# Kernel tuning notes

Hardware: AMD Instinct MI355X
Metric: run time of the kernel (lower is better)

## Reference

```python
import jax, jax.numpy as jnp
import numpy as np

NUM_GAUSS = 64
MAX_R = 5.0
ANG_TO_NM = 0.1  # du.ANG_TO_NM_SCALE
L = 4
C_NODE = 256
C_HID = 256
MAX_ATOMS = 100
B = 512      # building blocks
NPB = 32     # atoms per block
K = 20       # max_neighbors
N = B * NPB
E = N * K
GAUSS_COEFF = -0.5 / (MAX_R / (NUM_GAUSS - 1)) ** 2


def setup_inputs() -> dict:
    rng = np.random.default_rng(0)
    # all atoms of a block inside a 2.5A cube -> every pair within MAX_R=5A,
    # so radius_graph capped at K neighbors == K-nearest graph (fixed E).
    pos = (rng.random((B, NPB, 3)) * 2.5).astype(np.float32)
    d = np.linalg.norm(pos[:, :, None, :] - pos[:, None, :, :], axis=-1)  # [B,n,n]
    ii = np.arange(NPB)
    d[:, ii, ii] = np.inf  # loop=False
    nbr = np.argsort(d, axis=-1)[:, :, :K]  # [B,n,K] nearest neighbors
    base = (np.arange(B) * NPB)[:, None, None]
    row = np.broadcast_to(ii[None, :, None], (B, NPB, K)) + base
    col = nbr + base
    edge_index = np.stack([row.reshape(-1), col.reshape(-1)]).astype(np.int64)

    key = jax.random.key(0)
    ks = jax.random.split(key, 8)

    def lin(k, fi, fo):
        return jax.random.normal(k, (L, fi, fo), jnp.float32) / np.sqrt(fi).astype(np.float32)

    d_e_in = 2 * C_NODE + 1 + NUM_GAUSS  # 577
    return {
        'local_coords': jnp.asarray(pos.reshape(N, 3)),
        'atom_types': jax.random.randint(ks[0], (N,), 1, MAX_ATOMS + 1),  # 1..max_atoms
        'edge_index': jnp.asarray(edge_index),
        'batch_bb': jnp.repeat(jnp.arange(B, dtype=jnp.int32), NPB),
        'atom_embed': jax.random.normal(ks[1], (MAX_ATOMS, C_NODE), jnp.float32) * 0.1,
        'offset': jnp.linspace(0.0, MAX_R, NUM_GAUSS, dtype=jnp.float32),
        'We1': lin(ks[2], d_e_in, C_HID), 'be1': jnp.zeros((L, C_HID), jnp.float32),
        'We2': lin(ks[3], C_HID, C_HID), 'be2': jnp.zeros((L, C_HID), jnp.float32),
        'Wn1': lin(ks[4], C_HID + C_NODE, C_HID), 'bn1': jnp.zeros((L, C_HID), jnp.float32),
        'Wn2': lin(ks[5], C_HID, C_NODE), 'bn2': jnp.zeros((L, C_NODE), jnp.float32),
    }


def _forward(local_coords, atom_types, edge_index, batch_bb, atom_embed, offset,
             We1, be1, We2, be2, Wn1, bn1, Wn2, bn2):
    row, col = edge_index[0], edge_index[1]
    h = atom_embed[atom_types - 1]                      # [N, C_NODE]
    # Gaussian smearing of pairwise distances (Angstrom)
    dvec = local_coords[col] - local_coords[row]        # [E, 3]
    dist = jnp.sqrt(jnp.sum(dvec * dvec, axis=-1))      # [E]
    edge_attr = jnp.exp(GAUSS_COEFF * (dist[:, None] - offset[None, :]) ** 2)  # [E, 64]
    coord = local_coords * ANG_TO_NM
    cdiff = coord[row] - coord[col]
    radial = jnp.sum(cdiff * cdiff, axis=-1, keepdims=True)  # [E, 1]
    nblocks = batch_bb.shape[0] // NPB  # static
    for l in range(L):  # small fixed layer count
        e_in = jnp.concatenate([h[row], h[col], radial, edge_attr], axis=-1)  # [E, 577]
        m = jax.nn.relu(e_in @ We1[l] + be1[l])
        m = jax.nn.relu(m @ We2[l] + be2[l])                 # edge_mlp output [E, C_HID]
        agg = jax.ops.segment_sum(m, row, num_segments=N)    # scatter-sum to nodes
        n_in = jnp.concatenate([h, agg], axis=-1)            # [N, C_NODE + C_HID]
        out = jax.nn.relu(n_in @ Wn1[l] + bn1[l]) @ Wn2[l] + bn2[l]
        node_update = h + out                                # residual inside E_GCL
        h = h + node_update                                  # outer residual in forward
    # global_mean_pool over building blocks
    s = jax.ops.segment_sum(h, batch_bb, num_segments=B)
    cnt = jax.ops.segment_sum(jnp.ones((h.shape[0], 1), h.dtype), batch_bb, num_segments=B)
    return s / cnt


def reference(local_coords, atom_types, edge_index, batch_bb, atom_embed, offset,
              We1, be1, We2, be2, Wn1, bn1, Wn2, bn2):
    return _forward(local_coords, atom_types, edge_index, batch_bb, atom_embed, offset,
                    We1, be1, We2, be2, Wn1, bn1, Wn2, bn2)
```

## Files before the change

kernel.cpp:

```cpp
#include <hip/hip_runtime.h>
#include <hip/hip_bf16.h>
#include <stdint.h>

#define NATOMS 16384
#define ETOT   327680
#define NLAYER 4

typedef __hip_bfloat16 bf16;
using bf16x8 = __attribute__((ext_vector_type(8))) short;
using bf16x4 = __attribute__((ext_vector_type(4))) short;
using f32x4  = __attribute__((ext_vector_type(4))) float;

#define LDSF_STRIDE 260

__device__ __forceinline__ float bf2f(short s) {
  union { float f; unsigned u; } x; x.u = ((unsigned)(unsigned short)s) << 16; return x.f;
}
__device__ __forceinline__ short f2bf(float f) {
  bf16 b = __float2bfloat16(f);
  return *(short*)&b;
}

__device__ __forceinline__ void async16(const void* g, void* l) {
  __builtin_amdgcn_global_load_lds(
      (const __attribute__((address_space(1))) unsigned int*)g,
      (__attribute__((address_space(3))) unsigned int*)l, 16, 0, 0);
}

template<int KTOT, int EPI, int MT>
__global__ void __launch_bounds__(256, 2)
gemm_k(const bf16* A, const bf16* A2, const bf16* B,
       bf16* Obf, int ldOut, const float* bias,
       float* Hf, bf16* Hbf)
{
  __shared__ __align__(16) char smem[49152];
  const int tid  = threadIdx.x;
  const int w    = tid >> 6;
  const int lane = tid & 63;
  const int q    = lane >> 4;
  const int t16  = lane & 15;
  const size_t row0 = (size_t)blockIdx.x * MT;
  const int ncol0 = blockIdx.y * 256;
  constexpr int MI = MT / 16;
  constexpr int AI = MT / 32;

  f32x4 acc[MI][4] = {};
  constexpr int NCHUNK = KTOT / 64;
  for (int kc = 0; kc < NCHUNK; ++kc) {
    const int k0 = kc * 64;
    __syncthreads();
    #pragma unroll
    for (int ii = 0; ii < AI; ++ii) {
      int i = w * AI + ii;
      int f = i * 64 + lane;
      int m = f >> 3, s = f & 7;
      int ko = s ^ (m & 7);
      async16(A + (row0 + (size_t)m) * KTOT + (size_t)(k0 + ko * 8), smem + i * 1024);
    }
    #pragma unroll
    for (int ii = 0; ii < 8; ++ii) {
      int i = w * 8 + ii;
      int f = i * 64 + lane;
      int n = f >> 3, s = f & 7;
      int ko = s ^ (n & 7);
      async16(B + (size_t)(ncol0 + n) * KTOT + (size_t)(k0 + ko * 8),
              smem + 16384 + i * 1024);
    }
    __syncthreads();
    #pragma unroll
    for (int ks = 0; ks < 2; ++ks) {
      bf16x8 av[MI]; bf16x8 bv[4];
      const int ko = q + 4 * ks;
      #pragma unroll
      for (int mi = 0; mi < MI; ++mi) {
        int m = 16 * mi + t16;
        int f = m * 8 + (ko ^ (m & 7));
        av[mi] = *(const bf16x8*)(smem + f * 16);
      }
      #pragma unroll
      for (int ni = 0; ni < 4; ++ni) {
        int n = 64 * w + 16 * ni + t16;
        int f = n * 8 + (ko ^ (n & 7));
        bv[ni] = *(const bf16x8*)(smem + 16384 + f * 16);
      }
      #pragma unroll
      for (int mi = 0; mi < MI; ++mi)
        #pragma unroll
        for (int ni = 0; ni < 4; ++ni)
          acc[mi][ni] = __builtin_amdgcn_mfma_f32_16x16x32_bf16(
              av[mi], bv[ni], acc[mi][ni], 0, 0, 0);
    }
  }

  float* lds_f = (float*)smem;
  #pragma unroll
  for (int mi = 0; mi < MI; ++mi) {
    __syncthreads();
    #pragma unroll
    for (int ni = 0; ni < 4; ++ni)
      #pragma unroll
      for (int r = 0; r < 4; ++r)
        lds_f[(4 * q + r) * LDSF_STRIDE + 64 * w + 16 * ni + t16] = acc[mi][ni][r];
    __syncthreads();
    #pragma unroll
    for (int j = 0; j < 2; ++j) {
      int task = tid + 256 * j;
      int rr = task >> 5, cg = task & 31;
      int c0 = cg * 8;
      size_t rg = row0 + 16 * mi + rr;
      f32x4 v0 = *(const f32x4*)(lds_f + rr * LDSF_STRIDE + c0);
      f32x4 v1 = *(const f32x4*)(lds_f + rr * LDSF_STRIDE + c0 + 4);
      float v[8] = {v0[0], v0[1], v0[2], v0[3], v1[0], v1[1], v1[2], v1[3]};
      bf16x8 o;
      #pragma unroll
      for (int k = 0; k < 8; ++k) {
        float vv = v[k];
        if (bias != nullptr && ncol0 == 0) vv += bias[c0 + k];
        o[k] = f2bf(vv);
      }
      *(bf16x8*)(Obf + rg * ldOut + (ncol0 + c0)) = o;
    }
  }
}

#define WINC 40960
#define WINR 57856
#define SCOL 59968
#define SRAD 60288
#define WPITCH 528

__global__ void __launch_bounds__(256, 2)
edge_fused(const bf16* Wgp_l, const bf16* W2p_l, const float* off,
           const float* pos, const int* eidx, const bf16* Prc,
           const float* wrad, const float* be2, bf16* Agg)
{
  __shared__ __align__(16) char smem[60608];
  int*   s_col = (int*)  (smem + SCOL);
  float* s_rad = (float*)(smem + SRAD);

  const int tid  = threadIdx.x;
  const int w    = tid >> 6;
  const int lane = tid & 63;
  const int q    = lane >> 4;
  const int t16  = lane & 15;
  const int blk  = blockIdx.x;
  const int node0  = (blk >> 3) * 32;
  const int rnode0 = blk * 4;
  const int ebase  = blk * 80;

  bf16x8 wgf[4][2];
  #pragma unroll
  for (int fi = 0; fi < 4; ++fi)
    #pragma unroll
    for (int ks = 0; ks < 2; ++ks)
      wgf[fi][ks] = *(const bf16x8*)(Wgp_l + (size_t)(((fi * 2 + ks) * 4 + w) * 512)
                                     + lane * 8);

  {
    int row = tid >> 3, seg = tid & 7;
    const bf16* src = Prc + (size_t)(node0 + row) * 512 + 256 + seg * 32;
    char* dst = smem + WINC + row * WPITCH + seg * 64;
    #pragma unroll
    for (int j = 0; j < 4; ++j)
      *(bf16x8*)(dst + j * 16) = *(const bf16x8*)(src + j * 8);
  }
  if (tid < 128) {
    int row = tid >> 5, seg = tid & 31;
    *(bf16x8*)(smem + WINR + row * WPITCH + seg * 16) =
        *(const bf16x8*)(Prc + (size_t)(rnode0 + row) * 512 + seg * 8);
  }

  if (tid < 80) {
    int e = ebase + tid;
    int rg = rnode0 + tid / 20;
    int cg = eidx[ETOT + e];
    float dx = pos[cg * 3 + 0] - pos[rg * 3 + 0];
    float dy = pos[cg * 3 + 1] - pos[rg * 3 + 1];
    float dz = pos[cg * 3 + 2] - pos[rg * 3 + 2];
    float d2 = dx * dx + dy * dy + dz * dz;
    s_col[tid] = cg & 31;
    s_rad[tid] = 0.01f * d2;
    float d = sqrtf(d2);
    const float GC = -0.5f / ((5.0f / 63.0f) * (5.0f / 63.0f));
    #pragma unroll
    for (int oct = 0; oct < 8; ++oct) {
      bf16x8 v;
      #pragma unroll
      for (int j = 0; j < 8; ++j) {
        float t = d - off[oct * 8 + j];
        v[j] = f2bf(__expf(GC * t * t));
      }
      int f = tid * 8 + (oct ^ (tid & 7));
      *(bf16x8*)(smem + f * 16) = v;
    }
  }
  __syncthreads();

  f32x4 acc1[4][5] = {};
  #pragma unroll
  for (int ks = 0; ks < 2; ++ks) {
    const int ko = q + 4 * ks;
    bf16x8 gv[5];
    #pragma unroll
    for (int ci = 0; ci < 5; ++ci) {
      int e = 16 * ci + t16;
      int f = e * 8 + (ko ^ (e & 7));
      gv[ci] = *(const bf16x8*)(smem + f * 16);
    }
    #pragma unroll
    for (int fi = 0; fi < 4; ++fi)
      #pragma unroll
      for (int ci = 0; ci < 5; ++ci)
        acc1[fi][ci] = __builtin_amdgcn_mfma_f32_16x16x32_bf16(
            wgf[fi][ks], gv[ci], acc1[fi][ci], 0, 0, 0);
  }
  __syncthreads();

  {
    f32x4 tw[4];
    #pragma unroll
    for (int fi = 0; fi < 4; ++fi)
      tw[fi] = *(const f32x4*)(wrad + 64 * w + 16 * fi + 4 * q);
    #pragma unroll
    for (int ci = 0; ci < 5; ++ci) {
      int e = 16 * ci + t16;
      int rl = e / 20;
      int cl = s_col[e];
      float rad = s_rad[e];
      #pragma unroll
      for (int fi = 0; fi < 4; ++fi) {
        int fb = 64 * w + 16 * fi + 4 * q;
        bf16x4 pr = *(const bf16x4*)(smem + WINR + rl * WPITCH + fb * 2);
        bf16x4 pc = *(const bf16x4*)(smem + WINC + cl * WPITCH + fb * 2);
        bf16x4 o;
        #pragma unroll
        for (int r = 0; r < 4; ++r) {
          float val = acc1[fi][ci][r] + rad * tw[fi][r]
                    + bf2f(pr[r]) + bf2f(pc[r]);
          o[r] = f2bf(fmaxf(val, 0.f));
        }
        int u = (16 * w + 4 * fi + q) ^ (e & 14);
        *(bf16x4*)(smem + e * 512 + u * 8) = o;
      }
    }
  }
  __syncthreads();

  f32x4 acc2[5][4] = {};
  #pragma unroll
  for (int kc = 0; kc < 4; ++kc) {
    bf16x8 bv[4][2];
    #pragma unroll
    for (int ni = 0; ni < 4; ++ni)
      #pragma unroll
      for (int ks = 0; ks < 2; ++ks) {
        int frag = kc * 8 + ks * 4 + ni;
        bv[ni][ks] = *(const bf16x8*)(W2p_l + (size_t)((frag * 4 + w) * 512)
                                      + lane * 8);
      }
    #pragma unroll
    for (int ks = 0; ks < 2; ++ks) {
      const int ko = q + 4 * ks;
      bf16x8 av[5];
      #pragma unroll
      for (int mi = 0; mi < 5; ++mi) {
        int e = 16 * mi + t16;
        int ub = (2 * (8 * kc + ko)) ^ (t16 & 14);
        av[mi] = *(const bf16x8*)(smem + e * 512 + ub * 8);
      }
      #pragma unroll
      for (int mi = 0; mi < 5; ++mi)
        #pragma unroll
        for (int ni = 0; ni < 4; ++ni)
          acc2[mi][ni] = __builtin_amdgcn_mfma_f32_16x16x32_bf16(
              av[mi], bv[ni][ks], acc2[mi][ni], 0, 0, 0);
    }
  }

  #pragma unroll
  for (int ni = 0; ni < 4; ++ni) {
    float b = be2[64 * w + 16 * ni + t16];
    float pp[5];
    #pragma unroll
    for (int mi = 0; mi < 5; ++mi) {
      float s = 0.f;
      #pragma unroll
      for (int r = 0; r < 4; ++r) s += fmaxf(acc2[mi][ni][r] + b, 0.f);
      pp[mi] = s;
    }
    #pragma unroll
    for (int nn = 0; nn < 4; ++nn) {
      float s = 0.f;
      #pragma unroll
      for (int mi = 0; mi < 5; ++mi) {
        int g = 4 * mi + q;
        if (g >= 5 * nn && g <= 5 * nn + 4) s += pp[mi];
      }
      s += __shfl_xor(s, 16, 64);
      s += __shfl_xor(s, 32, 64);
      if (q == nn)
        Agg[(size_t)(rnode0 + nn) * 256 + 64 * w + 16 * ni + t16] =
            __float2bfloat16(s);
    }
  }
}

template<bool DO_PRC>
__global__ void __launch_bounds__(256, 2)
node_fused(const bf16* Hbf_in, const bf16* Agg, const bf16* Wn1p_l,
           const bf16* Wn2p_l, const bf16* Wrcp_n,
           const float* bn1, const float* bn2, const float* be1_n,
           float* Hf, bf16* Hbf, bf16* Prc)
{
  __shared__ __align__(16) char smem[49152];
  __shared__ float s_bn1[256];
  __shared__ float s_bn2[256];
  char* T = smem + 32768;
  float* lds_f = (float*)smem;

  const int tid  = threadIdx.x;
  const int w    = tid >> 6;
  const int lane = tid & 63;
  const int q    = lane >> 4;
  const int t16  = lane & 15;
  const size_t row0 = (size_t)blockIdx.x * 32;

  #pragma unroll
  for (int ii = 0; ii < 8; ++ii) {
    int i = w * 8 + ii;
    int ko = (lane & 56) | ((lane & 7) ^ (i & 7));
    const bf16* srcp = ((lane < 32) ? Hbf_in : Agg)
                     + (row0 + (size_t)i) * 256 + ((ko * 8) & 255);
    async16(srcp, smem + i * 1024);
  }
  s_bn1[tid] = bn1[tid];
  s_bn2[tid] = bn2[tid];
  __syncthreads();

  f32x4 acc1[4][2] = {};
  for (int kc = 0; kc < 8; ++kc) {
    #pragma unroll
    for (int ks = 0; ks < 2; ++ks) {
      const int ko = kc * 8 + q + 4 * ks;
      bf16x8 af[4];
      #pragma unroll
      for (int fi = 0; fi < 4; ++fi)
        af[fi] = *(const bf16x8*)(Wn1p_l +
                   (size_t)((fi * 16 + kc * 2 + ks) * 4 + w) * 512 + lane * 8);
      bf16x8 bv[2];
      #pragma unroll
      for (int ci = 0; ci < 2; ++ci) {
        int node = 16 * ci + t16;
        int sl = (ko & 56) | ((ko & 7) ^ (node & 7));
        bv[ci] = *(const bf16x8*)(smem + node * 1024 + sl * 16);
      }
      #pragma unroll
      for (int fi = 0; fi < 4; ++fi)
        #pragma unroll
        for (int ci = 0; ci < 2; ++ci)
          acc1[fi][ci] = __builtin_amdgcn_mfma_f32_16x16x32_bf16(
              af[fi], bv[ci], acc1[fi][ci], 0, 0, 0);
    }
  }

  #pragma unroll
  for (int ci = 0; ci < 2; ++ci) {
    int node = 16 * ci + t16;
    #pragma unroll
    for (int fi = 0; fi < 4; ++fi) {
      int fb = 64 * w + 16 * fi + 4 * q;
      f32x4 tb = *(const f32x4*)(s_bn1 + fb);
      bf16x4 o;
      #pragma unroll
      for (int r = 0; r < 4; ++r)
        o[r] = f2bf(fmaxf(acc1[fi][ci][r] + tb[r], 0.f));
      int u = (16 * w + 4 * fi + q) ^ (node & 14);
      *(bf16x4*)(T + node * 512 + u * 8) = o;
    }
  }
  __syncthreads();

  f32x4 acc2[2][4] = {};
  #pragma unroll
  for (int kc = 0; kc < 4; ++kc) {
    bf16x8 bv[4][2];
    #pragma unroll
    for (int ni = 0; ni < 4; ++ni)
      #pragma unroll
      for (int ks = 0; ks < 2; ++ks) {
        int frag = kc * 8 + ks * 4 + ni;
        bv[ni][ks] = *(const bf16x8*)(Wn2p_l + (size_t)((frag * 4 + w) * 512)
                                      + lane * 8);
      }
    #pragma unroll
    for (int ks = 0; ks < 2; ++ks) {
      const int ko = q + 4 * ks;
      bf16x8 av[2];
      #pragma unroll
      for (int mi = 0; mi < 2; ++mi) {
        int row = 16 * mi + t16;
        int ub = (2 * (8 * kc + ko)) ^ (t16 & 14);
        av[mi] = *(const bf16x8*)(T + row * 512 + ub * 8);
      }
      #pragma unroll
      for (int mi = 0; mi < 2; ++mi)
        #pragma unroll
        for (int ni = 0; ni < 4; ++ni)
          acc2[mi][ni] = __builtin_amdgcn_mfma_f32_16x16x32_bf16(
              av[mi], bv[ni][ks], acc2[mi][ni], 0, 0, 0);
    }
  }

  #pragma unroll
  for (int mi = 0; mi < 2; ++mi) {
    __syncthreads();
    #pragma unroll
    for (int ni = 0; ni < 4; ++ni)
      #pragma unroll
      for (int r = 0; r < 4; ++r)
        lds_f[(4 * q + r) * LDSF_STRIDE + 64 * w + 16 * ni + t16] = acc2[mi][ni][r];
    __syncthreads();
    #pragma unroll
    for (int j = 0; j < 2; ++j) {
      int task = tid + 256 * j;
      int rr = task >> 5, cg = task & 31;
      int c0 = cg * 8;
      int rl = 16 * mi + rr;
      size_t rg = row0 + rl;
      f32x4 v0 = *(const f32x4*)(lds_f + rr * LDSF_STRIDE + c0);
      f32x4 v1 = *(const f32x4*)(lds_f + rr * LDSF_STRIDE + c0 + 4);
      float v[8] = {v0[0], v0[1], v0[2], v0[3], v1[0], v1[1], v1[2], v1[3]};
      f32x4 h0 = *(const f32x4*)(Hf + rg * 256 + c0);
      f32x4 h1 = *(const f32x4*)(Hf + rg * 256 + c0 + 4);
      float hh[8] = {h0[0], h0[1], h0[2], h0[3], h1[0], h1[1], h1[2], h1[3]};
      bf16x8 o; f32x4 n0, n1;
      #pragma unroll
      for (int k = 0; k < 8; ++k) {
        float hn = 2.f * hh[k] + v[k] + s_bn2[c0 + k];
        o[k] = f2bf(hn);
        if (k < 4) n0[k] = hn; else n1[k - 4] = hn;
      }
      *(f32x4*)(Hf + rg * 256 + c0)     = n0;
      *(f32x4*)(Hf + rg * 256 + c0 + 4) = n1;
      *(bf16x8*)(Hbf + rg * 256 + c0) = o;
      int s = cg ^ ((rl >> 1) & 7);
      *(bf16x8*)(T + rl * 512 + s * 16) = o;
    }
  }

  if constexpr (DO_PRC) {
    __syncthreads();
    #pragma unroll
    for (int nh = 0; nh < 2; ++nh) {
      f32x4 acc3[2][4] = {};
      #pragma unroll
      for (int kc = 0; kc < 4; ++kc) {
        bf16x8 bv[4][2];
        #pragma unroll
        for (int ni = 0; ni < 4; ++ni)
          #pragma unroll
          for (int ks = 0; ks < 2; ++ks) {
            int frag = kc * 8 + ks * 4 + ni;
            bv[ni][ks] = *(const bf16x8*)(Wrcp_n + (size_t)nh * 65536 +
                                          (size_t)((frag * 4 + w) * 512) + lane * 8);
          }
        #pragma unroll
        for (int ks = 0; ks < 2; ++ks) {
          const int ko = q + 4 * ks;
          bf16x8 av[2];
          #pragma unroll
          for (int mi = 0; mi < 2; ++mi) {
            int row = 16 * mi + t16;
            int ub = (2 * (8 * kc + ko)) ^ (t16 & 14);
            av[mi] = *(const bf16x8*)(T + row * 512 + ub * 8);
          }
          #pragma unroll
          for (int mi = 0; mi < 2; ++mi)
            #pragma unroll
            for (int ni = 0; ni < 4; ++ni)
              acc3[mi][ni] = __builtin_amdgcn_mfma_f32_16x16x32_bf16(
                  av[mi], bv[ni][ks], acc3[mi][ni], 0, 0, 0);
        }
      }
      #pragma unroll
      for (int mi = 0; mi < 2; ++mi) {
        __syncthreads();
        #pragma unroll
        for (int ni = 0; ni < 4; ++ni)
          #pragma unroll
          for (int r = 0; r < 4; ++r)
            lds_f[(4 * q + r) * LDSF_STRIDE + 64 * w + 16 * ni + t16] = acc3[mi][ni][r];
        __syncthreads();
        #pragma unroll
        for (int j = 0; j < 2; ++j) {
          int task = tid + 256 * j;
          int rr = task >> 5, cg = task & 31;
          int c0 = cg * 8;
          size_t rg = row0 + 16 * mi + rr;
          f32x4 v0 = *(const f32x4*)(lds_f + rr * LDSF_STRIDE + c0);
          f32x4 v1 = *(const f32x4*)(lds_f + rr * LDSF_STRIDE + c0 + 4);
          float v[8] = {v0[0], v0[1], v0[2], v0[3], v1[0], v1[1], v1[2], v1[3]};
          bf16x8 o;
          #pragma unroll
          for (int k = 0; k < 8; ++k) {
            float vv = v[k];
            if (nh == 0) vv += be1_n[c0 + k];
            o[k] = f2bf(vv);
          }
          *(bf16x8*)(Prc + rg * 512 + nh * 256 + c0) = o;
        }
      }
    }
  }
}

__global__ void wrct_kernel(const float* We1, bf16* WrcT) {
  int idx = blockIdx.x * 256 + threadIdx.x;
  int k = idx & 255, np = (idx >> 8) & 511;
  float v = (np < 256)
      ? We1[((size_t)k) * 256 + np]
      : We1[((size_t)256 + k) * 256 + (np - 256)];
  WrcT[idx] = __float2bfloat16(v);
}
__global__ void wgp_kernel(const float* We1, bf16* Wgp) {
  int idx = blockIdx.x * 256 + threadIdx.x;
  int i = idx & 16383, l = idx >> 14;
  int j = i & 7, lane = (i >> 3) & 63, w = (i >> 9) & 3, fr = i >> 11;
  int fi = fr >> 1, ks = fr & 1;
  int t16 = lane & 15, q = lane >> 4;
  int g = (q + 4 * ks) * 8 + j;
  int feat = 64 * w + 16 * fi + t16;
  Wgp[idx] = __float2bfloat16(We1[((size_t)l * 577 + 513 + g) * 256 + feat]);
}
__global__ void w2p_kernel(const float* W, bf16* Wp) {
  int idx = blockIdx.x * 256 + threadIdx.x;
  int i = idx & 65535, l = idx >> 16;
  int j = i & 7, lane = (i >> 3) & 63, w = (i >> 9) & 3, fr = i >> 11;
  int ni = fr & 3, ks = (fr >> 2) & 1, kc = fr >> 3;
  int t16 = lane & 15, q = lane >> 4;
  int k = kc * 64 + (q + 4 * ks) * 8 + j;
  int n = 64 * w + 16 * ni + t16;
  Wp[idx] = __float2bfloat16(W[((size_t)l * 256 + k) * 256 + n]);
}
__global__ void wrcp_kernel(const float* We1, bf16* Wrcp) {
  int idx = blockIdx.x * 256 + threadIdx.x;
  int i = idx & 65535, nh = (idx >> 16) & 1, l = idx >> 17;
  int j = i & 7, lane = (i >> 3) & 63, w = (i >> 9) & 3, fr = i >> 11;
  int ni = fr & 3, ks = (fr >> 2) & 1, kc = fr >> 3;
  int t16 = lane & 15, q = lane >> 4;
  int k = kc * 64 + (q + 4 * ks) * 8 + j;
  int n = 64 * w + 16 * ni + t16;
  Wrcp[idx] = __float2bfloat16(We1[((size_t)l * 577 + nh * 256 + k) * 256 + n]);
}
__global__ void wn1p_kernel(const float* Wn1, bf16* Wn1p) {
  int idx = blockIdx.x * 256 + threadIdx.x;
  int i = idx & 131071, l = idx >> 17;
  int j = i & 7, lane = (i >> 3) & 63, w = (i >> 9) & 3, fr = i >> 11;
  int fi = fr >> 4, kc = (fr & 15) >> 1, ks = fr & 1;
  int t16 = lane & 15, q = lane >> 4;
  int feat = 64 * w + 16 * fi + t16;
  int k = kc * 64 + (q + 4 * ks) * 8 + j;
  Wn1p[idx] = __float2bfloat16(Wn1[((size_t)l * 512 + k) * 256 + feat]);
}
__global__ void wrad_kernel(const float* We1, float* wrad) {
  int idx = blockIdx.x * 256 + threadIdx.x;
  int n = idx & 255, l = idx >> 8;
  wrad[idx] = We1[((size_t)l * 577 + 512) * 256 + n];
}

__global__ void h0_kernel(const int* types, const float* emb, float* h, bf16* hbf) {
  int i = blockIdx.x, c = threadIdx.x;
  float v = emb[(size_t)(types[i] - 1) * 256 + c];
  h[(size_t)i * 256 + c] = v;
  hbf[(size_t)i * 256 + c] = __float2bfloat16(v);
}

__global__ void pool_kernel(const float* h, float* out) {
  int b = blockIdx.x, c = threadIdx.x;
  float s = 0.f;
  #pragma unroll
  for (int j = 0; j < 32; ++j) s += h[((size_t)b * 32 + j) * 256 + c];
  out[(size_t)b * 256 + c] = s * (1.0f / 32.0f);
}

extern "C" void kernel_launch(void* const* d_in, const int* in_sizes, int n_in,
                              void* d_out, int out_size, void* d_ws, size_t ws_size,
                              hipStream_t stream) {
  const float* pos   = (const float*)d_in[0];
  const int*   atype = (const int*)  d_in[1];
  const int*   eidx  = (const int*)  d_in[2];
  const float* emb   = (const float*)d_in[4];
  const float* off   = (const float*)d_in[5];
  const float* We1   = (const float*)d_in[6];
  const float* be1   = (const float*)d_in[7];
  const float* We2   = (const float*)d_in[8];
  const float* be2   = (const float*)d_in[9];
  const float* Wn1   = (const float*)d_in[10];
  const float* bn1   = (const float*)d_in[11];
  const float* Wn2   = (const float*)d_in[12];
  const float* bn2   = (const float*)d_in[13];
  float* out = (float*)d_out;

  size_t o = 0;
  auto carve = [&](size_t bytes) {
    void* p = (char*)d_ws + o;
    o += (bytes + 255) & ~(size_t)255;
    return p;
  };
  float* h     = (float*)carve((size_t)NATOMS * 256 * 4);
  bf16*  hbf   = (bf16*) carve((size_t)NATOMS * 256 * 2);
  bf16*  Prc   = (bf16*) carve((size_t)NATOMS * 512 * 2);
  bf16*  aggbf = (bf16*) carve((size_t)NATOMS * 256 * 2);
  bf16*  WrcT  = (bf16*) carve((size_t)512 * 256 * 2);
  bf16*  Wgp   = (bf16*) carve((size_t)NLAYER * 16384 * 2);
  bf16*  W2p   = (bf16*) carve((size_t)NLAYER * 65536 * 2);
  bf16*  Wn1p  = (bf16*) carve((size_t)NLAYER * 131072 * 2);
  bf16*  Wn2p  = (bf16*) carve((size_t)NLAYER * 65536 * 2);
  bf16*  Wrcp  = (bf16*) carve((size_t)NLAYER * 2 * 65536 * 2);
  float* wradp = (float*)carve((size_t)NLAYER * 256 * 4);

  wrct_kernel<<< 512, 256, 0, stream>>>(We1, WrcT);
  wgp_kernel <<< 256, 256, 0, stream>>>(We1, Wgp);
  w2p_kernel <<<1024, 256, 0, stream>>>(We2, W2p);
  w2p_kernel <<<1024, 256, 0, stream>>>(Wn2, Wn2p);
  wrcp_kernel<<<2048, 256, 0, stream>>>(We1, Wrcp);
  wn1p_kernel<<<2048, 256, 0, stream>>>(Wn1, Wn1p);
  wrad_kernel<<<   4, 256, 0, stream>>>(We1, wradp);
  h0_kernel  <<<NATOMS, 256, 0, stream>>>(atype, emb, h, hbf);

  gemm_k<256, 0, 64><<<dim3(256, 2), 256, 0, stream>>>(
      hbf, nullptr, WrcT, Prc, 512, be1, nullptr, nullptr);

  for (int l = 0; l < NLAYER; ++l) {
    edge_fused<<<ETOT / 80, 256, 0, stream>>>(
        Wgp + (size_t)l * 16384, W2p + (size_t)l * 65536, off, pos,
        eidx, Prc, wradp + l * 256, be2 + l * 256, aggbf);
    if (l < NLAYER - 1) {
      node_fused<true><<<512, 256, 0, stream>>>(
          hbf, aggbf, Wn1p + (size_t)l * 131072, Wn2p + (size_t)l * 65536,
          Wrcp + (size_t)(l + 1) * 131072, bn1 + l * 256, bn2 + l * 256,
          be1 + (l + 1) * 256, h, hbf, Prc);
    } else {
      node_fused<false><<<512, 256, 0, stream>>>(
          hbf, aggbf, Wn1p + (size_t)l * 131072, Wn2p + (size_t)l * 65536,
          nullptr, bn1 + l * 256, bn2 + l * 256, nullptr, h, hbf, nullptr);
    }
  }

  pool_kernel<<<512, 256, 0, stream>>>(h, out);
}
```

Baseline: 581.4 us.

## Split edge kernel into two 40-edge halves to halve LDS and raise occupancy

The edge kernel now processes its 80 edges in two halves of 40, shrinking the shared-memory footprint from about 60KB to about 40KB and raising launch bounds from 2 to 4 blocks per CU. Gaussian smearing is computed directly in registers from a stored distance instead of being staged through LDS. Weight fragments are reloaded per half. The intent is more waves per CU to hide latency, at the cost of padded MFMA tiles (48 rows for 40 edges), duplicated weight loads and extra exp work. Tighter register limits may also cause spills.

```diff
diff --git a/kernel.cpp b/kernel.cpp
--- a/kernel.cpp
+++ b/kernel.cpp
@@ -123,20 +123,22 @@
   }
 }
 
-#define WINC 40960
-#define WINR 57856
-#define SCOL 59968
-#define SRAD 60288
+#define EWINC  20480
+#define EWINR  37376
+#define ESCOL  39488
+#define ESRAD  39808
+#define ESDIST 40128
 #define WPITCH 528
 
-__global__ void __launch_bounds__(256, 2)
+__global__ void __launch_bounds__(256, 4)
 edge_fused(const bf16* Wgp_l, const bf16* W2p_l, const float* off,
            const float* pos, const int* eidx, const bf16* Prc,
            const float* wrad, const float* be2, bf16* Agg)
 {
-  __shared__ __align__(16) char smem[60608];
-  int*   s_col = (int*)  (smem + SCOL);
-  float* s_rad = (float*)(smem + SRAD);
+  __shared__ __align__(16) char smem[40448];
+  int*   s_col  = (int*)  (smem + ESCOL);
+  float* s_rad  = (float*)(smem + ESRAD);
+  float* s_dist = (float*)(smem + ESDIST);
 
   const int tid  = threadIdx.x;
   const int w    = tid >> 6;
@@ -148,28 +150,19 @@
   const int rnode0 = blk * 4;
   const int ebase  = blk * 80;
 
-  bf16x8 wgf[4][2];
-  #pragma unroll
-  for (int fi = 0; fi < 4; ++fi)
-    #pragma unroll
-    for (int ks = 0; ks < 2; ++ks)
-      wgf[fi][ks] = *(const bf16x8*)(Wgp_l + (size_t)(((fi * 2 + ks) * 4 + w) * 512)
-                                     + lane * 8);
-
   {
     int row = tid >> 3, seg = tid & 7;
     const bf16* src = Prc + (size_t)(node0 + row) * 512 + 256 + seg * 32;
-    char* dst = smem + WINC + row * WPITCH + seg * 64;
+    char* dst = smem + EWINC + row * WPITCH + seg * 64;
     #pragma unroll
     for (int j = 0; j < 4; ++j)
       *(bf16x8*)(dst + j * 16) = *(const bf16x8*)(src + j * 8);
   }
   if (tid < 128) {
     int row = tid >> 5, seg = tid & 31;
-    *(bf16x8*)(smem + WINR + row * WPITCH + seg * 16) =
+    *(bf16x8*)(smem + EWINR + row * WPITCH + seg * 16) =
         *(const bf16x8*)(Prc + (size_t)(rnode0 + row) * 512 + seg * 8);
   }
-
   if (tid < 80) {
     int e = ebase + tid;
     int rg = rnode0 + tid / 20;
@@ -178,129 +171,143 @@
     float dy = pos[cg * 3 + 1] - pos[rg * 3 + 1];
     float dz = pos[cg * 3 + 2] - pos[rg * 3 + 2];
     float d2 = dx * dx + dy * dy + dz * dz;
-    s_col[tid] = cg & 31;
-    s_rad[tid] = 0.01f * d2;
-    float d = sqrtf(d2);
-    const float GC = -0.5f / ((5.0f / 63.0f) * (5.0f / 63.0f));
-    #pragma unroll
-    for (int oct = 0; oct < 8; ++oct) {
-      bf16x8 v;
-      #pragma unroll
-      for (int j = 0; j < 8; ++j) {
-        float t = d - off[oct * 8 + j];
-        v[j] = f2bf(__expf(GC * t * t));
-      }
-      int f = tid * 8 + (oct ^ (tid & 7));
-      *(bf16x8*)(smem + f * 16) = v;
-    }
-  }
-  __syncthreads();
-
-  f32x4 acc1[4][5] = {};
+    s_col[tid]  = cg & 31;
+    s_rad[tid]  = 0.01f * d2;
+    s_dist[tid] = sqrtf(d2);
+  }
+  float offk[2][8];
   #pragma unroll
   for (int ks = 0; ks < 2; ++ks) {
-    const int ko = q + 4 * ks;
-    bf16x8 gv[5];
-    #pragma unroll
-    for (int ci = 0; ci < 5; ++ci) {
-      int e = 16 * ci + t16;
-      int f = e * 8 + (ko ^ (e & 7));
-      gv[ci] = *(const bf16x8*)(smem + f * 16);
-    }
+    f32x4 o0 = *(const f32x4*)(off + (q + 4 * ks) * 8);
+    f32x4 o1 = *(const f32x4*)(off + (q + 4 * ks) * 8 + 4);
+    #pragma unroll
+    for (int j = 0; j < 4; ++j) { offk[ks][j] = o0[j]; offk[ks][4 + j] = o1[j]; }
+  }
+  __syncthreads();
+
+  const float GC = -0.5f / ((5.0f / 63.0f) * (5.0f / 63.0f));
+
+  for (int half = 0; half < 2; ++half) {
+    bf16x8 wgf[4][2];
     #pragma unroll
     for (int fi = 0; fi < 4; ++fi)
       #pragma unroll
-      for (int ci = 0; ci < 5; ++ci)
-        acc1[fi][ci] = __builtin_amdgcn_mfma_f32_16x16x32_bf16(
-            wgf[fi][ks], gv[ci], acc1[fi][ci], 0, 0, 0);
-  }
-  __syncthreads();
-
-  {
-    f32x4 tw[4];
-    #pragma unroll
-    for (int fi = 0; fi < 4; ++fi)
-      tw[fi] = *(const f32x4*)(wrad + 64 * w + 16 * fi + 4 * q);
-    #pragma unroll
-    for (int ci = 0; ci < 5; ++ci) {
-      int e = 16 * ci + t16;
-      int rl = e / 20;
-      int cl = s_col[e];
-      float rad = s_rad[e];
-      #pragma unroll
-      for (int fi = 0; fi < 4; ++fi) {
-        int fb = 64 * w + 16 * fi + 4 * q;
-        bf16x4 pr = *(const bf16x4*)(smem + WINR + rl * WPITCH + fb * 2);
-        bf16x4 pc = *(const bf16x4*)(smem + WINC + cl * WPITCH + fb * 2);
-        bf16x4 o;
-        #pragma unroll
-        for (int r = 0; r < 4; ++r) {
-          float val = acc1[fi][ci][r] + rad * tw[fi][r]
-                    + bf2f(pr[r]) + bf2f(pc[r]);
-          o[r] = f2bf(fmaxf(val, 0.f));
+      for (int ks = 0; ks < 2; ++ks)
+        wgf[fi][ks] = *(const bf16x8*)(Wgp_l +
+                        (size_t)(((fi * 2 + ks) * 4 + w) * 512) + lane * 8);
+
+    f32x4 acc1[4][3] = {};
+    #pragma unroll
+    for (int ci = 0; ci < 3; ++ci) {
+      int e = 40 * half + 16 * ci + t16;
+      float d = s_dist[e < 80 ? (e < 40 * half + 40 ? e : 40 * half) : 0];
+      bf16x8 gv[2];
+      #pragma unroll
+      for (int ks = 0; ks < 2; ++ks)
+        #pragma unroll
+        for (int j = 0; j < 8; ++j) {
+          float t = d - offk[ks][j];
+          gv[ks][j] = f2bf(__expf(GC * t * t));
         }
-        int u = (16 * w + 4 * fi + q) ^ (e & 14);
-        *(bf16x4*)(smem + e * 512 + u * 8) = o;
-      }
-    }
-  }
-  __syncthreads();
-
-  f32x4 acc2[5][4] = {};
-  #pragma unroll
-  for (int kc = 0; kc < 4; ++kc) {
-    bf16x8 bv[4][2];
-    #pragma unroll
-    for (int ni = 0; ni < 4; ++ni)
+      #pragma unroll
+      for (int ks = 0; ks < 2; ++ks)
+        #pragma unroll
+        for (int fi = 0; fi < 4; ++fi)
+          acc1[fi][ci] = __builtin_amdgcn_mfma_f32_16x16x32_bf16(
+              wgf[fi][ks], gv[ks], acc1[fi][ci], 0, 0, 0);
+    }
+
+    if (half) __syncthreads();
+
+    {
+      f32x4 tw[4];
+      #pragma unroll
+      for (int fi = 0; fi < 4; ++fi)
+        tw[fi] = *(const f32x4*)(wrad + 64 * w + 16 * fi + 4 * q);
+      #pragma unroll
+      for (int ci = 0; ci < 3; ++ci) {
+        int hr = 16 * ci + t16;
+        if (hr < 40) {
+          int e = 40 * half + hr;
+          int rl = e / 20;
+          int cl = s_col[e];
+          float rad = s_rad[e];
+          #pragma unroll
+          for (int fi = 0; fi < 4; ++fi) {
+            int fb = 64 * w + 16 * fi + 4 * q;
+            bf16x4 pr = *(const bf16x4*)(smem + EWINR + rl * WPITCH + fb * 2);
+            bf16x4 pc = *(const bf16x4*)(smem + EWINC + cl * WPITCH + fb * 2);
+            bf16x4 o;
+            #pragma unroll
+            for (int r = 0; r < 4; ++r) {
+              float val = acc1[fi][ci][r] + rad * tw[fi][r]
+                        + bf2f(pr[r]) + bf2f(pc[r]);
+              o[r] = f2bf(fmaxf(val, 0.f));
+            }
+            int u = (16 * w + 4 * fi + q) ^ (hr & 14);
+            *(bf16x4*)(smem + hr * 512 + u * 8) = o;
+          }
+        }
+      }
+    }
+    __syncthreads();
+
+    f32x4 acc2[3][4] = {};
+    #pragma unroll
+    for (int kc = 0; kc < 4; ++kc) {
+      bf16x8 bv[4][2];
+      #pragma unroll
+      for (int ni = 0; ni < 4; ++ni)
+        #pragma unroll
+        for (int ks = 0; ks < 2; ++ks) {
+          int frag = kc * 8 + ks * 4 + ni;
+          bv[ni][ks] = *(const bf16x8*)(W2p_l + (size_t)((frag * 4 + w) * 512)
+                                        + lane * 8);
+        }
       #pragma unroll
       for (int ks = 0; ks < 2; ++ks) {
-        int frag = kc * 8 + ks * 4 + ni;
-        bv[ni][ks] = *(const bf16x8*)(W2p_l + (size_t)((frag * 4 + w) * 512)
-                                      + lane * 8);
-      }
-    #pragma unroll
-    for (int ks = 0; ks < 2; ++ks) {
-      const int ko = q + 4 * ks;
-      bf16x8 av[5];
-      #pragma unroll
-      for (int mi = 0; mi < 5; ++mi) {
-        int e = 16 * mi + t16;
-        int ub = (2 * (8 * kc + ko)) ^ (t16 & 14);
-        av[mi] = *(const bf16x8*)(smem + e * 512 + ub * 8);
-      }
-      #pragma unroll
-      for (int mi = 0; mi < 5; ++mi)
-        #pragma unroll
-        for (int ni = 0; ni < 4; ++ni)
-          acc2[mi][ni] = __builtin_amdgcn_mfma_f32_16x16x32_bf16(
-              av[mi], bv[ni][ks], acc2[mi][ni], 0, 0, 0);
-    }
-  }
-
-  #pragma unroll
-  for (int ni = 0; ni < 4; ++ni) {
-    float b = be2[64 * w + 16 * ni + t16];
-    float pp[5];
-    #pragma unroll
-    for (int mi = 0; mi < 5; ++mi) {
-      float s = 0.f;
-      #pragma unroll
-      for (int r = 0; r < 4; ++r) s += fmaxf(acc2[mi][ni][r] + b, 0.f);
-      pp[mi] = s;
-    }
-    #pragma unroll
-    for (int nn = 0; nn < 4; ++nn) {
-      float s = 0.f;
-      #pragma unroll
-      for (int mi = 0; mi < 5; ++mi) {
-        int g = 4 * mi + q;
-        if (g >= 5 * nn && g <= 5 * nn + 4) s += pp[mi];
-      }
-      s += __shfl_xor(s, 16, 64);
-      s += __shfl_xor(s, 32, 64);
-      if (q == nn)
-        Agg[(size_t)(rnode0 + nn) * 256 + 64 * w + 16 * ni + t16] =
-            __float2bfloat16(s);
+        const int ko = q + 4 * ks;
+        bf16x8 av[3];
+        #pragma unroll
+        for (int mi = 0; mi < 3; ++mi) {
+          int row = 16 * mi + t16;
+          int ub = (2 * (8 * kc + ko)) ^ (t16 & 14);
+          av[mi] = *(const bf16x8*)(smem + row * 512 + ub * 8);
+        }
+        #pragma unroll
+        for (int mi = 0; mi < 3; ++mi)
+          #pragma unroll
+          for (int ni = 0; ni < 4; ++ni)
+            acc2[mi][ni] = __builtin_amdgcn_mfma_f32_16x16x32_bf16(
+                av[mi], bv[ni][ks], acc2[mi][ni], 0, 0, 0);
+      }
+    }
+
+    #pragma unroll
+    for (int ni = 0; ni < 4; ++ni) {
+      float b = be2[64 * w + 16 * ni + t16];
+      float pp[3];
+      #pragma unroll
+      for (int mi = 0; mi < 3; ++mi) {
+        float s = 0.f;
+        #pragma unroll
+        for (int r = 0; r < 4; ++r) s += fmaxf(acc2[mi][ni][r] + b, 0.f);
+        pp[mi] = s;
+      }
+      #pragma unroll
+      for (int nn = 0; nn < 2; ++nn) {
+        float s = 0.f;
+        #pragma unroll
+        for (int mi = 0; mi < 3; ++mi) {
+          int g = 4 * mi + q;
+          if (g >= 5 * nn && g <= 5 * nn + 4) s += pp[mi];
+        }
+        s += __shfl_xor(s, 16, 64);
+        s += __shfl_xor(s, 32, 64);
+        if (q == nn)
+          Agg[(size_t)(rnode0 + 2 * half + nn) * 256 + 64 * w + 16 * ni + t16] =
+              __float2bfloat16(s);
+      }
     }
   }
 }
```

Result: slower. 1.072 ms (+84.3%).
